# Optimization experiments

Measured on AMD Instinct MI355X. Metric: run time of the kernel, lower is better.

## Reference

```python
import jax, jax.numpy as jnp
import numpy as np

SCALE = 0.08838834764831845  # 1/sqrt(128)
SOFT_CAP = 0.0               # module default soft_cap=0 -> disabled


def setup_inputs() -> dict:
    key = jax.random.key(0)
    k1, k2, k3, k4, k5 = jax.random.split(key, 5)
    R, B, Hq, Hk, Dq, Dv = 4, 16, 32, 8, 128, 128
    P, PAGE, M = 8192, 1, 2048  # pages per rank, page_size, max pages per seq
    q = jax.random.normal(k1, (B, Hq, Dq), dtype=jnp.float16)
    k_cache = jax.random.normal(k2, (R, P, PAGE, Hk, Dq), dtype=jnp.float16)
    v_cache = jax.random.normal(k3, (R, P, PAGE, Hk, Dv), dtype=jnp.float16)
    # at least 1 valid token per rank per sequence
    global_kv_lens = jax.random.randint(k4, (R, B), 1, M * PAGE + 1, dtype=jnp.int32)
    block_table = jax.random.randint(k5, (R, B, M), 0, P, dtype=jnp.int32)
    return {"q": q, "k_cache": k_cache, "v_cache": v_cache,
            "global_kv_lens": global_kv_lens, "block_table": block_table}


def _flash_decode(q, k_cache, v_cache, global_kv_lens, block_table):
    R, P, PAGE, Hk, Dq = k_cache.shape
    B, Hq, _ = q.shape
    G = Hq // Hk                      # GQA group size
    M = block_table.shape[-1]
    K = M * PAGE                      # max kv tokens per rank per seq
    Dv = v_cache.shape[-1]

    # paged gather per rank: kc[bt] -> [B, M, PAGE, Hk, D]
    kg = jax.vmap(lambda kc, bt: kc[bt])(k_cache, block_table)
    vg = jax.vmap(lambda vc, bt: vc[bt])(v_cache, block_table)
    kg = kg.reshape(R, B, K, Hk, Dq).astype(jnp.float32)
    vg = vg.reshape(R, B, K, Hk, Dv).astype(jnp.float32)

    qf = q.astype(jnp.float32).reshape(B, Hk, G, Dq)
    # scores [R, B, Hk, G, K]
    s = jnp.einsum('bhgd,rbkhd->rbhgk', qf, kg) * SCALE
    if SOFT_CAP > 0:
        s = SOFT_CAP * jnp.tanh(s / SOFT_CAP)

    valid = jnp.arange(K)[None, None, :] < global_kv_lens[:, :, None]  # [R,B,K]
    s = jnp.where(valid[:, :, None, None, :], s, -jnp.inf)

    # per-rank partial softmax stats (what gqa_local_kernels_fused produces)
    m = jnp.max(s, axis=-1)                      # [R,B,Hk,G]
    p = jnp.exp(s - m[..., None])
    l = jnp.sum(p, axis=-1)                      # [R,B,Hk,G]
    o = jnp.einsum('rbhgk,rbkhd->rbhgd', p, vg)  # [R,B,Hk,G,Dv]

    # cross-rank lse-weighted reduce (gqa_global_reduce_fused)
    m_g = jnp.max(m, axis=0)                     # [B,Hk,G]
    w = jnp.exp(m - m_g[None])                   # [R,B,Hk,G]
    o_tot = jnp.sum(w[..., None] * o, axis=0)    # [B,Hk,G,Dv]
    l_tot = jnp.sum(w * l, axis=0)               # [B,Hk,G]
    out = (o_tot / l_tot[..., None]).reshape(B, Hq, Dv)
    return out.astype(jnp.float32)


def reference(q, k_cache, v_cache, global_kv_lens, block_table):
    return _flash_decode(q, k_cache, v_cache, global_kv_lens, block_table)
```

## Files before the change

### kernel.cpp

```cpp
#include <hip/hip_runtime.h>
#include <math.h>


typedef float f32x4 __attribute__((ext_vector_type(4)));

#define R_ 4
#define B_ 16
#define HQ_ 32
#define HK_ 8
#define G_ 4
#define D_ 128
#define P_ 8192
#define M_ 2048
#define HKD (HK_ * D_)
#define NR 8
#define NBK 256
#define PROW 2560
#define SC2 (0.08838834764831845f * 1.4426950408889634f)
#define MNEG (-1.0e30f)

__device__ __forceinline__ int clampP(int p) {
  return p < 0 ? 0 : (p >= P_ ? P_ - 1 : p);
}

__global__ __launch_bounds__(256) void fd_compact(
    const int* __restrict__ lens, const int* __restrict__ bt,
    unsigned* __restrict__ ws_pages, int* __restrict__ ws_meta) {
  __shared__ int hist[NBK];
  __shared__ int cur[NBK];
  __shared__ int rstart[NR + 1], rcnt[NR];
  const int rb = blockIdx.x;
  const int tid = threadIdx.x;
  int kvlen = lens[rb];
  kvlen = kvlen < 0 ? 0 : (kvlen > M_ ? M_ : kvlen);
  const int* btrow = bt + rb * M_;

  for (int i = tid; i < NBK; i += 256) hist[i] = 0;
  __syncthreads();
  for (int t = tid; t < kvlen; t += 256)
    atomicAdd(&hist[clampP(btrow[t]) >> 5], 1);
  __syncthreads();
  if (tid == 0) {
    int pos = 0;
    for (int s = 0; s < NR; ++s) {
      rstart[s] = pos;
      int n = 0;
      for (int j = 0; j < NBK / NR; ++j) {
        cur[s * (NBK / NR) + j] = pos + n;
        n += hist[s * (NBK / NR) + j];
      }
      rcnt[s] = n;
      pos += (n + 63) & ~63;
    }
    rstart[NR] = pos;
  }
  __syncthreads();
  unsigned* prow = ws_pages + (size_t)rb * PROW;
  for (int t = tid; t < kvlen; t += 256) {
    const int p = clampP(btrow[t]);
    const int d = atomicAdd(&cur[p >> 5], 1);
    prow[d] = ((unsigned)p) << 12;
  }
  __syncthreads();
  for (int s = 0; s < NR; ++s) {
    const int from = rstart[s] + rcnt[s];
    const int to = rstart[s + 1];
    for (int i = from + tid; i < to; i += 256)
      prow[i] = ((unsigned)(s * (P_ / NR))) << 12;
  }
  if (tid < NR) {
    ws_meta[rb * 2 * NR + tid * 2] = rstart[tid];
    ws_meta[rb * 2 * NR + tid * 2 + 1] = rcnt[tid];
  }
}

__global__ __launch_bounds__(256) void fd_partial(
    const float* __restrict__ q, const float* __restrict__ kc,
    const float* __restrict__ vc, const unsigned* __restrict__ ws_pages,
    const int* __restrict__ ws_meta, float* __restrict__ ws_m,
    float* __restrict__ ws_l, float* __restrict__ ws_o) {
  const int bid = blockIdx.x;
  const int s = bid >> 9;
  const int rbh = bid & 511;
  const int hk = rbh & (HK_ - 1);
  const int rb = rbh >> 3;
  const int b = rb & (B_ - 1);
  const int r = rb >> 4;
  const int rec = bid;

  const int lane = threadIdx.x & 63;
  const int w = threadIdx.x >> 6;
  const int tg = lane >> 4;
  const int ds = (lane & 15) * 8;
  const unsigned dsb = ds * 4u;

  const int start = ws_meta[rb * 2 * NR + s * 2];
  const int n = ws_meta[rb * 2 * NR + s * 2 + 1];
  if (n <= 0) {
    if (lane == 0) ws_m[rec * G_ + w] = MNEG;
    return;
  }

  float qf[G_][8];
  {
    const float* qp = q + (size_t)(b * HQ_ + hk * G_) * D_ + ds;
#pragma unroll
    for (int h = 0; h < G_; ++h) {
      const f32x4* p = (const f32x4*)(qp + h * D_);
      f32x4 a = p[0], c = p[1];
#pragma unroll
      for (int j = 0; j < 4; ++j) {
        qf[h][j] = a[j] * SC2;
        qf[h][4 + j] = c[j] * SC2;
      }
    }
  }

  const unsigned* plist = ws_pages + (size_t)rb * PROW + start;
  const float* kb = kc + (size_t)r * P_ * HKD + (size_t)hk * D_;
  const float* vb = vc + (size_t)r * P_ * HKD + (size_t)hk * D_;

  float m[G_], l[G_], acc[G_][8];
#pragma unroll
  for (int h = 0; h < G_; ++h) {
    m[h] = MNEG;
    l[h] = 0.f;
#pragma unroll
    for (int j = 0; j < 8; ++j) acc[h][j] = 0.f;
  }

  const int nIt = (n + 63) >> 6;
  const int sbase = w * 16 + tg * 4;

  uint4 pgN = *(const uint4*)(plist + sbase);

#pragma unroll 1
  for (int i = 0; i < nIt; ++i) {
    const uint4 pg = pgN;
    if (i + 1 < nIt) pgN = *(const uint4*)(plist + sbase + (i + 1) * 64);
    const unsigned o0 = pg.x + dsb;
    const unsigned o1 = pg.y + dsb;
    const unsigned o2 = pg.z + dsb;
    const unsigned o3 = pg.w + dsb;

    float k0[8], k1[8], k2[8], k3[8], v0[8], v1[8], v2[8], v3[8];
    {
      const char* kcb = (const char*)kb;
      const char* vcb = (const char*)vb;
      const f32x4* p;
      p = (const f32x4*)(kcb + o0);
#pragma unroll
      for (int j = 0; j < 4; ++j) { k0[j] = p[0][j]; k0[4 + j] = p[1][j]; }
      p = (const f32x4*)(kcb + o1);
#pragma unroll
      for (int j = 0; j < 4; ++j) { k1[j] = p[0][j]; k1[4 + j] = p[1][j]; }
      p = (const f32x4*)(kcb + o2);
#pragma unroll
      for (int j = 0; j < 4; ++j) { k2[j] = p[0][j]; k2[4 + j] = p[1][j]; }
      p = (const f32x4*)(kcb + o3);
#pragma unroll
      for (int j = 0; j < 4; ++j) { k3[j] = p[0][j]; k3[4 + j] = p[1][j]; }
      p = (const f32x4*)(vcb + o0);
#pragma unroll
      for (int j = 0; j < 4; ++j) { v0[j] = p[0][j]; v0[4 + j] = p[1][j]; }
      p = (const f32x4*)(vcb + o1);
#pragma unroll
      for (int j = 0; j < 4; ++j) { v1[j] = p[0][j]; v1[4 + j] = p[1][j]; }
      p = (const f32x4*)(vcb + o2);
#pragma unroll
      for (int j = 0; j < 4; ++j) { v2[j] = p[0][j]; v2[4 + j] = p[1][j]; }
      p = (const f32x4*)(vcb + o3);
#pragma unroll
      for (int j = 0; j < 4; ++j) { v3[j] = p[0][j]; v3[4 + j] = p[1][j]; }
    }

    float d0[G_], d1[G_], d2[G_], d3[G_];
#pragma unroll
    for (int h = 0; h < G_; ++h) {
      float a0 = 0.f, a1 = 0.f, a2 = 0.f, a3 = 0.f;
#pragma unroll
      for (int j = 0; j < 8; ++j) {
        a0 += qf[h][j] * k0[j];
        a1 += qf[h][j] * k1[j];
        a2 += qf[h][j] * k2[j];
        a3 += qf[h][j] * k3[j];
      }
      d0[h] = a0; d1[h] = a1; d2[h] = a2; d3[h] = a3;
    }
#pragma unroll
    for (int msk = 1; msk <= 8; msk <<= 1) {
#pragma unroll
      for (int h = 0; h < G_; ++h) {
        d0[h] += __shfl_xor(d0[h], msk);
        d1[h] += __shfl_xor(d1[h], msk);
        d2[h] += __shfl_xor(d2[h], msk);
        d3[h] += __shfl_xor(d3[h], msk);
      }
    }

    const int tb = sbase + i * 64;
    const bool va0 = tb < n;
    const bool va1 = tb + 1 < n;
    const bool va2 = tb + 2 < n;
    const bool va3 = tb + 3 < n;
#pragma unroll
    for (int h = 0; h < G_; ++h) {
      const float s0 = va0 ? d0[h] : -INFINITY;
      const float s1 = va1 ? d1[h] : -INFINITY;
      const float s2 = va2 ? d2[h] : -INFINITY;
      const float s3 = va3 ? d3[h] : -INFINITY;
      const float mt = fmaxf(fmaxf(s0, s1), fmaxf(s2, s3));
      const float mn = fmaxf(m[h], mt);
      const float sc = exp2f(m[h] - mn);
      const float p0 = exp2f(s0 - mn);
      const float p1 = exp2f(s1 - mn);
      const float p2 = exp2f(s2 - mn);
      const float p3 = exp2f(s3 - mn);
      m[h] = mn;
      l[h] = l[h] * sc + (p0 + p1) + (p2 + p3);
#pragma unroll
      for (int j = 0; j < 8; ++j)
        acc[h][j] = acc[h][j] * sc + p0 * v0[j] + p1 * v1[j] + p2 * v2[j] +
                    p3 * v3[j];
    }
  }

#pragma unroll
  for (int h = 0; h < G_; ++h) {
#pragma unroll
    for (int off = 16; off <= 32; off <<= 1) {
      const float mo = __shfl_xor(m[h], off);
      const float lo = __shfl_xor(l[h], off);
      float ao[8];
#pragma unroll
      for (int j = 0; j < 8; ++j) ao[j] = __shfl_xor(acc[h][j], off);
      const float mn = fmaxf(m[h], mo);
      const float se = exp2f(m[h] - mn);
      const float so_ = exp2f(mo - mn);
      l[h] = l[h] * se + lo * so_;
#pragma unroll
      for (int j = 0; j < 8; ++j) acc[h][j] = acc[h][j] * se + ao[j] * so_;
      m[h] = mn;
    }
  }

  __shared__ float sm[4][G_], sl[4][G_], so[4][G_][D_ + 4];
  if (lane < 16) {
#pragma unroll
    for (int h = 0; h < G_; ++h) {
#pragma unroll
      for (int j = 0; j < 8; ++j) so[w][h][ds + j] = acc[h][j];
    }
    if (lane == 0) {
#pragma unroll
      for (int h = 0; h < G_; ++h) {
        sm[w][h] = m[h];
        sl[w][h] = l[h];
      }
    }
  }
  __syncthreads();

  const int g = w;
  const float mw0 = sm[0][g], mw1 = sm[1][g], mw2 = sm[2][g], mw3 = sm[3][g];
  const float mf = fmaxf(fmaxf(mw0, mw1), fmaxf(mw2, mw3));
  const float wt0 = exp2f(mw0 - mf);
  const float wt1 = exp2f(mw1 - mf);
  const float wt2 = exp2f(mw2 - mf);
  const float wt3 = exp2f(mw3 - mf);
  const float lf =
      wt0 * sl[0][g] + wt1 * sl[1][g] + wt2 * sl[2][g] + wt3 * sl[3][g];
  const float of0 = wt0 * so[0][g][lane] + wt1 * so[1][g][lane] +
                    wt2 * so[2][g][lane] + wt3 * so[3][g][lane];
  const float of1 = wt0 * so[0][g][lane + 64] + wt1 * so[1][g][lane + 64] +
                    wt2 * so[2][g][lane + 64] + wt3 * so[3][g][lane + 64];
  ws_o[((size_t)rec * G_ + g) * D_ + lane] = of0;
  ws_o[((size_t)rec * G_ + g) * D_ + lane + 64] = of1;
  if (lane == 0) {
    ws_m[rec * G_ + g] = mf;
    ws_l[rec * G_ + g] = lf;
  }
}

__global__ __launch_bounds__(128) void fd_reduce(
    const float* __restrict__ ws_m, const float* __restrict__ ws_l,
    const float* __restrict__ ws_o, float* __restrict__ out) {
  const int row = blockIdx.x;
  const int g = row % G_;
  const int hk = (row / G_) % HK_;
  const int b = row / (G_ * HK_);
  const int d = threadIdx.x;

  float mf = MNEG;
  for (int r = 0; r < R_; ++r)
    for (int s = 0; s < NR; ++s) {
      const int rec = s * 512 + (r * B_ + b) * HK_ + hk;
      mf = fmaxf(mf, ws_m[rec * G_ + g]);
    }
  float of = 0.f, lf = 0.f;
  for (int r = 0; r < R_; ++r)
    for (int s = 0; s < NR; ++s) {
      const int rec = s * 512 + (r * B_ + b) * HK_ + hk;
      const float wt = exp2f(ws_m[rec * G_ + g] - mf);
      of += wt * ws_o[((size_t)rec * G_ + g) * D_ + d];
      lf += wt * ws_l[rec * G_ + g];
    }
  out[(size_t)(b * HQ_ + hk * G_ + g) * D_ + d] = of / lf;
}

__device__ __forceinline__ void load8u(const float* __restrict__ ubase,
                                       unsigned boff, float o[8]) {
  const f32x4* p = (const f32x4*)((const char*)ubase + boff);
  f32x4 a = p[0];
  f32x4 b = p[1];
#pragma unroll
  for (int j = 0; j < 4; ++j) { o[j] = a[j]; o[4 + j] = b[j]; }
}

__global__ __launch_bounds__(256) void fd_mono(
    const float* __restrict__ q, const float* __restrict__ kc,
    const float* __restrict__ vc, const int* __restrict__ lens,
    const int* __restrict__ bt, float* __restrict__ out) {
  const int hk = blockIdx.x % HK_;
  const int b = blockIdx.x / HK_;
  const int lane = threadIdx.x & 63;
  const int g = threadIdx.x >> 6;
  const int tg = lane >> 4;
  const int ds = (lane & 15) * 8;
  const unsigned dsb = ds * 4u;

  float qf[8];
  load8u(q + (size_t)(b * HQ_ + hk * G_ + g) * D_ + ds, 0u, qf);
#pragma unroll
  for (int j = 0; j < 8; ++j) qf[j] *= SC2;

  float m = MNEG, l = 0.f, acc[8];
#pragma unroll
  for (int j = 0; j < 8; ++j) acc[j] = 0.f;

  for (int r = 0; r < R_; ++r) {
    int kvlen = lens[r * B_ + b];
    if (kvlen < 0) kvlen = 0;
    if (kvlen > M_) kvlen = M_;
    const int* btrow = bt + (r * B_ + b) * M_;
    const float* kb = kc + (size_t)r * P_ * HKD + (size_t)hk * D_;
    const float* vb = vc + (size_t)r * P_ * HKD + (size_t)hk * D_;

#pragma unroll 1
    for (int t = 0; t < kvlen; t += 4) {
      const int ta = t + tg;
      const bool va = ta < kvlen;
      const unsigned oa = ((unsigned)clampP(btrow[va ? ta : 0]) << 12) + dsb;
      float ka[8], wa[8];
      load8u(kb, oa, ka);
      load8u(vb, oa, wa);

      float da = 0.f;
#pragma unroll
      for (int j = 0; j < 8; ++j) da += qf[j] * ka[j];
#pragma unroll
      for (int msk = 1; msk <= 8; msk <<= 1) da += __shfl_xor(da, msk);

      const float sa = va ? da : -INFINITY;
      const float mn = fmaxf(m, sa);
      const float sc = exp2f(m - mn);
      const float pa = exp2f(sa - mn);
      m = mn;
      l = l * sc + pa;
#pragma unroll
      for (int j = 0; j < 8; ++j) acc[j] = acc[j] * sc + pa * wa[j];
    }
  }

#pragma unroll
  for (int off = 16; off <= 32; off <<= 1) {
    const float mo = __shfl_xor(m, off);
    const float lo = __shfl_xor(l, off);
    float ao[8];
#pragma unroll
    for (int j = 0; j < 8; ++j) ao[j] = __shfl_xor(acc[j], off);
    const float mn = fmaxf(m, mo);
    const float se = exp2f(m - mn);
    const float so_ = exp2f(mo - mn);
    l = l * se + lo * so_;
#pragma unroll
    for (int j = 0; j < 8; ++j) acc[j] = acc[j] * se + ao[j] * so_;
    m = mn;
  }

  if (lane < 16) {
    float inv = (l > 0.f) ? 1.0f / l : 0.f;
#pragma unroll
    for (int j = 0; j < 8; ++j)
      out[(size_t)(b * HQ_ + hk * G_ + g) * D_ + ds + j] = acc[j] * inv;
  }
}

extern "C" void kernel_launch(void* const* d_in, const int* in_sizes, int n_in,
                              void* d_out, int out_size, void* d_ws,
                              size_t ws_size, hipStream_t stream) {
  const float* q = (const float*)d_in[0];
  const float* kc = (const float*)d_in[1];
  const float* vc = (const float*)d_in[2];
  const int* lens = (const int*)d_in[3];
  const int* bt = (const int*)d_in[4];
  float* out = (float*)d_out;

  const int nrec = NR * R_ * B_ * HK_;
  const size_t sz_pages = (size_t)R_ * B_ * PROW * 4;
  const size_t sz_meta = (size_t)R_ * B_ * 2 * NR * 4;
  const size_t sz_ml = (size_t)nrec * G_ * 4;
  const size_t sz_o = (size_t)nrec * G_ * D_ * 4;
  const size_t need = sz_pages + sz_meta + 2 * sz_ml + sz_o;

  if (need <= ws_size) {
    char* p = (char*)d_ws;
    unsigned* ws_pages = (unsigned*)p;          p += sz_pages;
    int* ws_meta = (int*)p;                     p += sz_meta;
    float* ws_m = (float*)p;                    p += sz_ml;
    float* ws_l = (float*)p;                    p += sz_ml;
    float* ws_o = (float*)p;
    fd_compact<<<R_ * B_, 256, 0, stream>>>(lens, bt, ws_pages, ws_meta);
    fd_partial<<<nrec, 256, 0, stream>>>(q, kc, vc, ws_pages, ws_meta, ws_m,
                                         ws_l, ws_o);
    fd_reduce<<<B_ * HK_ * G_, 128, 0, stream>>>(ws_m, ws_l, ws_o, out);
  } else {
    fd_mono<<<B_ * HK_, 256, 0, stream>>>(q, kc, vc, lens, bt, out);
  }
}
```

Before: 100.6 us.

## Split sorted page list into equal-count chunks across sixteen splits

The compaction kernel now does a full counting sort of each sequence's pages by page bucket and pads the tail with the last page, with no per-split metadata. The partial kernel derives each split's range from the kv length, giving each of the now sixteen splits an equal, four-aligned share of tokens. This replaces the earlier page-range splits, which padded every split to 64 and could be unbalanced. It doubles the number of partial blocks and records for the reduce kernel to combine, in exchange for more parallelism and even work per block.

```diff
diff --git a/kernel.cpp b/kernel.cpp
--- a/kernel.cpp
+++ b/kernel.cpp
@@ -13,9 +13,9 @@
 #define P_ 8192
 #define M_ 2048
 #define HKD (HK_ * D_)
-#define NR 8
+#define NR 16
 #define NBK 256
-#define PROW 2560
+#define PROW 2112
 #define SC2 (0.08838834764831845f * 1.4426950408889634f)
 #define MNEG (-1.0e30f)
 
@@ -25,14 +25,13 @@
 
 __global__ __launch_bounds__(256) void fd_compact(
     const int* __restrict__ lens, const int* __restrict__ bt,
-    unsigned* __restrict__ ws_pages, int* __restrict__ ws_meta) {
+    unsigned* __restrict__ ws_pages) {
   __shared__ int hist[NBK];
   __shared__ int cur[NBK];
-  __shared__ int rstart[NR + 1], rcnt[NR];
   const int rb = blockIdx.x;
   const int tid = threadIdx.x;
   int kvlen = lens[rb];
-  kvlen = kvlen < 0 ? 0 : (kvlen > M_ ? M_ : kvlen);
+  kvlen = kvlen < 1 ? 1 : (kvlen > M_ ? M_ : kvlen);
   const int* btrow = bt + rb * M_;
 
   for (int i = tid; i < NBK; i += 256) hist[i] = 0;
@@ -42,17 +41,10 @@
   __syncthreads();
   if (tid == 0) {
     int pos = 0;
-    for (int s = 0; s < NR; ++s) {
-      rstart[s] = pos;
-      int n = 0;
-      for (int j = 0; j < NBK / NR; ++j) {
-        cur[s * (NBK / NR) + j] = pos + n;
-        n += hist[s * (NBK / NR) + j];
-      }
-      rcnt[s] = n;
-      pos += (n + 63) & ~63;
-    }
-    rstart[NR] = pos;
+    for (int j = 0; j < NBK; ++j) {
+      cur[j] = pos;
+      pos += hist[j];
+    }
   }
   __syncthreads();
   unsigned* prow = ws_pages + (size_t)rb * PROW;
@@ -62,22 +54,14 @@
     prow[d] = ((unsigned)p) << 12;
   }
   __syncthreads();
-  for (int s = 0; s < NR; ++s) {
-    const int from = rstart[s] + rcnt[s];
-    const int to = rstart[s + 1];
-    for (int i = from + tid; i < to; i += 256)
-      prow[i] = ((unsigned)(s * (P_ / NR))) << 12;
-  }
-  if (tid < NR) {
-    ws_meta[rb * 2 * NR + tid * 2] = rstart[tid];
-    ws_meta[rb * 2 * NR + tid * 2 + 1] = rcnt[tid];
-  }
+  const unsigned last = prow[kvlen - 1];
+  for (int i = kvlen + tid; i < PROW; i += 256) prow[i] = last;
 }
 
 __global__ __launch_bounds__(256) void fd_partial(
     const float* __restrict__ q, const float* __restrict__ kc,
-    const float* __restrict__ vc, const unsigned* __restrict__ ws_pages,
-    const int* __restrict__ ws_meta, float* __restrict__ ws_m,
+    const float* __restrict__ vc, const int* __restrict__ lens,
+    const unsigned* __restrict__ ws_pages, float* __restrict__ ws_m,
     float* __restrict__ ws_l, float* __restrict__ ws_o) {
   const int bid = blockIdx.x;
   const int s = bid >> 9;
@@ -94,12 +78,16 @@
   const int ds = (lane & 15) * 8;
   const unsigned dsb = ds * 4u;
 
-  const int start = ws_meta[rb * 2 * NR + s * 2];
-  const int n = ws_meta[rb * 2 * NR + s * 2 + 1];
-  if (n <= 0) {
+  int kvlen = lens[rb];
+  kvlen = kvlen < 1 ? 1 : (kvlen > M_ ? M_ : kvlen);
+  const int qn = (((kvlen + NR - 1) / NR) + 3) & ~3;
+  const int start = s * qn;
+  int nc = kvlen - start;
+  if (nc <= 0) {
     if (lane == 0) ws_m[rec * G_ + w] = MNEG;
     return;
   }
+  if (nc > qn) nc = qn;
 
   float qf[G_][8];
   {
@@ -129,7 +117,7 @@
     for (int j = 0; j < 8; ++j) acc[h][j] = 0.f;
   }
 
-  const int nIt = (n + 63) >> 6;
+  const int nIt = (nc + 63) >> 6;
   const int sbase = w * 16 + tg * 4;
 
   uint4 pgN = *(const uint4*)(plist + sbase);
@@ -199,10 +187,10 @@
     }
 
     const int tb = sbase + i * 64;
-    const bool va0 = tb < n;
-    const bool va1 = tb + 1 < n;
-    const bool va2 = tb + 2 < n;
-    const bool va3 = tb + 3 < n;
+    const bool va0 = tb < nc;
+    const bool va1 = tb + 1 < nc;
+    const bool va2 = tb + 2 < nc;
+    const bool va3 = tb + 3 < nc;
 #pragma unroll
     for (int h = 0; h < G_; ++h) {
       const float s0 = va0 ? d0[h] : -INFINITY;
@@ -408,20 +396,18 @@
 
   const int nrec = NR * R_ * B_ * HK_;
   const size_t sz_pages = (size_t)R_ * B_ * PROW * 4;
-  const size_t sz_meta = (size_t)R_ * B_ * 2 * NR * 4;
   const size_t sz_ml = (size_t)nrec * G_ * 4;
   const size_t sz_o = (size_t)nrec * G_ * D_ * 4;
-  const size_t need = sz_pages + sz_meta + 2 * sz_ml + sz_o;
+  const size_t need = sz_pages + 2 * sz_ml + sz_o;
 
   if (need <= ws_size) {
     char* p = (char*)d_ws;
-    unsigned* ws_pages = (unsigned*)p;          p += sz_pages;
-    int* ws_meta = (int*)p;                     p += sz_meta;
-    float* ws_m = (float*)p;                    p += sz_ml;
-    float* ws_l = (float*)p;                    p += sz_ml;
+    unsigned* ws_pages = (unsigned*)p;  p += sz_pages;
+    float* ws_m = (float*)p;            p += sz_ml;
+    float* ws_l = (float*)p;            p += sz_ml;
     float* ws_o = (float*)p;
-    fd_compact<<<R_ * B_, 256, 0, stream>>>(lens, bt, ws_pages, ws_meta);
-    fd_partial<<<nrec, 256, 0, stream>>>(q, kc, vc, ws_pages, ws_meta, ws_m,
+    fd_compact<<<R_ * B_, 256, 0, stream>>>(lens, bt, ws_pages);
+    fd_partial<<<nrec, 256, 0, stream>>>(q, kc, vc, lens, ws_pages, ws_m,
                                          ws_l, ws_o);
     fd_reduce<<<B_ * HK_ * G_, 128, 0, stream>>>(ws_m, ws_l, ws_o, out);
   } else {
```

After: 133.2 us. 1.32x slower.
